# Performance work log

Measured on AMD Instinct MI355X. Metric: run time of the kernel, lower is better.

Reference implementation:

```python
import jax, jax.numpy as jnp
import numpy as np

N_TOKEN = 267735
CUTOFFS = [20000, 40000, 200000, N_TOKEN]  # includes final n_token
D_EMBED = 1024
D_PROJ = 1024
DIV_VAL = 4
N = 1024  # number of tokens


def setup_inputs() -> dict:
    key = jax.random.key(0)
    ks = jax.random.split(key, 20)
    inp = {}
    inp['hidden'] = jax.random.normal(ks[0], (N, D_PROJ), dtype=jnp.float32)
    inp['target'] = jax.random.randint(ks[1], (N,), 0, N_TOKEN, dtype=jnp.int64)
    cutoff_ends = [0] + CUTOFFS
    # per-cluster params: weight [vocab_i, d_emb_i], bias [vocab_i], proj [d_proj, d_emb_i]
    for i in range(4):
        l, r = cutoff_ends[i], cutoff_ends[i + 1]
        d_i = D_EMBED // (DIV_VAL ** i)
        s = 1.0 / np.sqrt(d_i)
        inp[f'W{i}'] = jax.random.uniform(ks[2 + 3 * i], (r - l, d_i), minval=-s, maxval=s, dtype=jnp.float32)
        inp[f'b{i}'] = jnp.zeros((r - l,), dtype=jnp.float32)
        inp[f'proj{i}'] = jax.random.uniform(ks[3 + 3 * i], (D_PROJ, d_i), minval=-s, maxval=s, dtype=jnp.float32)
    inp['cluster_W'] = jax.random.normal(ks[15], (3, D_EMBED), dtype=jnp.float32) * 0.02
    inp['cluster_b'] = jnp.zeros((3,), dtype=jnp.float32)
    return inp


def _adaptive_nll(hidden, target, W0, b0, proj0, W1, b1, proj1, W2, b2, proj2, W3, b3, proj3, cluster_W, cluster_b):
    cutoff_ends = [0] + CUTOFFS
    # head: shortlist vocab + 3 cluster logits
    head_w = jnp.concatenate([W0, cluster_W], axis=0)          # [20003, d_embed]
    head_b = jnp.concatenate([b0, cluster_b], axis=0)          # [20003]
    head_logit = (hidden @ proj0) @ head_w.T + head_b          # [N, 20003]
    head_lp = jax.nn.log_softmax(head_logit, axis=1)
    # shortlist cluster (i == 0)
    t0 = jnp.clip(target, 0, cutoff_ends[1] - 1)
    lp0 = jnp.take_along_axis(head_lp, t0[:, None], axis=1)[:, 0]
    m0 = target < cutoff_ends[1]
    nll = jnp.where(m0, -lp0, 0.0)
    # tail clusters; faithful to original: head column is head_lp[:, -i]
    tails = [(W1, b1, proj1), (W2, b2, proj2), (W3, b3, proj3)]
    for i, (W_i, b_i, proj_i) in enumerate(tails, start=1):
        l, r = cutoff_ends[i], cutoff_ends[i + 1]
        tail_logit = (hidden @ proj_i) @ W_i.T + b_i           # [N, r-l]
        tail_lp = jax.nn.log_softmax(tail_logit, axis=1)
        ti = jnp.clip(target - l, 0, r - l - 1)
        lp_tail = jnp.take_along_axis(tail_lp, ti[:, None], axis=1)[:, 0]
        lp_i = head_lp[:, -i] + lp_tail
        m_i = (target >= l) & (target < r)
        nll = nll + jnp.where(m_i, -lp_i, 0.0)
    return nll.mean()  # reduction='mean'


def reference(hidden, target, W0, b0, proj0, W1, b1, proj1, W2, b2, proj2, W3, b3, proj3, cluster_W, cluster_b):
    return _adaptive_nll(hidden, target, W0, b0, proj0, W1, b1, proj1, W2, b2, proj2, W3, b3, proj3, cluster_W, cluster_b)
```

## Files before the change

### kernel.cpp

```cpp
#include <hip/hip_runtime.h>
#include <stdint.h>


typedef __attribute__((ext_vector_type(8))) short short8;
typedef __attribute__((ext_vector_type(4))) float f32x4;

__device__ __forceinline__ float bf2f(unsigned short u) {
    union { unsigned int i; float f; } v; v.i = ((unsigned int)u) << 16; return v.f;
}
__device__ __forceinline__ unsigned short f2bf(float f) {
    union { float f; unsigned int i; } v; v.f = f;
    unsigned int u = v.i;
    return (unsigned short)((u + 0x7fffu + ((u >> 16) & 1u)) >> 16);
}
__device__ __forceinline__ float wave_sum(float v) {
    v += __shfl_xor(v, 1, 64);  v += __shfl_xor(v, 2, 64);
    v += __shfl_xor(v, 4, 64);  v += __shfl_xor(v, 8, 64);
    v += __shfl_xor(v, 16, 64); v += __shfl_xor(v, 32, 64);
    return v;
}
__device__ __forceinline__ short8 pack8(float4 a, float4 b) {
    union { int4 i; short8 s; } r;
    r.i.x = __builtin_amdgcn_perm(__float_as_uint(a.y), __float_as_uint(a.x), 0x07060302u);
    r.i.y = __builtin_amdgcn_perm(__float_as_uint(a.w), __float_as_uint(a.z), 0x07060302u);
    r.i.z = __builtin_amdgcn_perm(__float_as_uint(b.y), __float_as_uint(b.x), 0x07060302u);
    r.i.w = __builtin_amdgcn_perm(__float_as_uint(b.w), __float_as_uint(b.z), 0x07060302u);
    return r.s;
}

__device__ __forceinline__ void dev_transpose(int bx, int by,
                                              const float* __restrict__ src,
                                              unsigned short* __restrict__ dst,
                                              int K, int N) {
    __shared__ unsigned short tile[32][33];
    int k0 = by * 32, n0 = bx * 32;
    int tx = threadIdx.x & 31, ty = threadIdx.x >> 5;
#pragma unroll
    for (int j = 0; j < 4; ++j) {
        int k = k0 + ty + j * 8, n = n0 + tx;
        float v = (n < N) ? src[(size_t)k * N + n] : 0.f;
        tile[ty + j * 8][tx] = f2bf(v);
    }
    __syncthreads();
#pragma unroll
    for (int j = 0; j < 4; ++j) {
        int n = n0 + ty + j * 8, k = k0 + tx;
        if (n < N) dst[(size_t)n * K + k] = tile[tx][ty + j * 8];
    }
}

__device__ __forceinline__ void dev_biasfill(int bid, const float* __restrict__ b,
                                             float* __restrict__ bp, int vocab, int padded) {
    int i = bid * 256 + threadIdx.x;
    if (i < padded) bp[i] = (i < vocab) ? b[i] : -1e30f;
}

__global__ __launch_bounds__(256)
void k_pre(const float* __restrict__ hidden, unsigned short* __restrict__ hid_bf,
           const float* __restrict__ proj0, unsigned short* __restrict__ pT0,
           const float* __restrict__ proj1, unsigned short* __restrict__ pT1,
           const float* __restrict__ proj2, unsigned short* __restrict__ pT2,
           const float* __restrict__ proj3, unsigned short* __restrict__ pT3,
           const float* __restrict__ b0, float* __restrict__ b0p,
           const float* __restrict__ b1, float* __restrict__ b1p,
           const float* __restrict__ b2, float* __restrict__ b2p,
           const float* __restrict__ b3, float* __restrict__ b3p) {
    int bid = blockIdx.x, tid = threadIdx.x;
    if (bid < 1024) {
        int i = bid * 256 + tid;
        float4 v = ((const float4*)hidden)[i];
        ushort4 o;
        o.x = f2bf(v.x); o.y = f2bf(v.y); o.z = f2bf(v.z); o.w = f2bf(v.w);
        ((ushort4*)hid_bf)[i] = o;
    }
    else if (bid < 2048) { int i = bid - 1024; dev_transpose(i & 31, i >> 5, proj0, pT0, 1024, 1024); }
    else if (bid < 2304) { int i = bid - 2048; dev_transpose(i & 7,  i >> 3, proj1, pT1, 1024, 256); }
    else if (bid < 2368) { int i = bid - 2304; dev_transpose(i & 1,  i >> 1, proj2, pT2, 1024, 64); }
    else if (bid < 2400) { int i = bid - 2368; dev_transpose(0,      i,      proj3, pT3, 1024, 16); }
    else if (bid < 2479) dev_biasfill(bid - 2400, b0, b0p, 20000, 20096);
    else if (bid < 2558) dev_biasfill(bid - 2479, b1, b1p, 20000, 20096);
    else if (bid < 3188) dev_biasfill(bid - 2558, b2, b2p, 160000, 161280);
    else                 dev_biasfill(bid - 3188, b3, b3p, 67735, 69632);
}

template <int NK32, int KD>
__device__ __forceinline__ void dev_convw(int bid, const float* __restrict__ W,
                                          unsigned short* __restrict__ Wf,
                                          int vocab, int upad) {
    int u = bid * 4 + (threadIdx.x >> 6);
    if (u >= upad) return;
    int lane = threadIdx.x & 63, q = lane >> 4, ln = lane & 15;
    int row = u * 16 + ln;
    bool rv = row < vocab;
    const float* src = W + (size_t)row * KD;
#pragma unroll
    for (int ks = 0; ks < NK32; ++ks) {
        int k0 = ks * 32 + q * 8;
        float4 a = {0.f, 0.f, 0.f, 0.f}, b = {0.f, 0.f, 0.f, 0.f};
        if (rv && k0 < KD) {
            a = *(const float4*)(src + k0);
            b = *(const float4*)(src + k0 + 4);
        }
        *(short8*)(Wf + ((size_t)u * NK32 + ks) * 512 + lane * 8) = pack8(a, b);
    }
}

#define BM 128
#define BN 128
#define BK 64
#define LDT 72
template <int NK32O>
__device__ __forceinline__ void dev_gemm(unsigned short* __restrict__ ls,
                                         int bx, int by,
                                         const unsigned short* __restrict__ A, int lda,
                                         const unsigned short* __restrict__ B, int ldb,
                                         unsigned short* __restrict__ Cf,
                                         int N, int K) {
    unsigned short* lsA = ls;
    unsigned short* lsB = ls + BM * LDT;
    int tid = threadIdx.x;
    int mBase = bx * BM, nBase = by * BN;
    int wid = tid >> 6, lane = tid & 63;
    int wr = wid >> 1, wc = wid & 1;
    int q = lane >> 4, ln = lane & 15;
    f32x4 acc[4][4] = {};

    for (int k0 = 0; k0 < K; k0 += BK) {
        __syncthreads();
        int ch = tid & 7;
#pragma unroll
        for (int p = 0; p < 4; ++p) {
            int r = p * 32 + (tid >> 3);
            *(uint4*)(&lsA[r * LDT + ch * 8]) =
                *(const uint4*)(A + (size_t)(mBase + r) * lda + k0 + ch * 8);
        }
#pragma unroll
        for (int p = 0; p < 4; ++p) {
            int r = p * 32 + (tid >> 3);
            uint4 v = {0u, 0u, 0u, 0u};
            if (nBase + r < N)
                v = *(const uint4*)(B + (size_t)(nBase + r) * ldb + k0 + ch * 8);
            *(uint4*)(&lsB[r * LDT + ch * 8]) = v;
        }
        __syncthreads();
#pragma unroll
        for (int ks = 0; ks < 2; ++ks) {
            short8 af[4], bfr[4];
#pragma unroll
            for (int mi = 0; mi < 4; ++mi)
                af[mi] = *(const short8*)(&lsA[(wr * 64 + mi * 16 + ln) * LDT + ks * 32 + q * 8]);
#pragma unroll
            for (int ni = 0; ni < 4; ++ni)
                bfr[ni] = *(const short8*)(&lsB[(wc * 64 + ni * 16 + ln) * LDT + ks * 32 + q * 8]);
#pragma unroll
            for (int mi = 0; mi < 4; ++mi)
#pragma unroll
                for (int ni = 0; ni < 4; ++ni)
                    acc[mi][ni] = __builtin_amdgcn_mfma_f32_16x16x32_bf16(
                        af[mi], bfr[ni], acc[mi][ni], 0, 0, 0);
        }
    }
#pragma unroll
    for (int ni = 0; ni < 4; ++ni) {
        int col = nBase + wc * 64 + ni * 16 + ln;
        if (col < N) {
            int k32 = col >> 5, qc = (col >> 3) & 3, j = col & 7;
#pragma unroll
            for (int mi = 0; mi < 4; ++mi) {
                int m16 = (mBase >> 4) + wr * 4 + mi;
                size_t base = ((size_t)m16 * NK32O + k32) * 512 + (size_t)qc * 128 + j;
#pragma unroll
                for (int r = 0; r < 4; ++r) {
                    int mrem = q * 4 + r;
                    Cf[base + mrem * 8] = f2bf(acc[mi][ni][r]);
                }
            }
        }
    }
}

__global__ __launch_bounds__(256)
void k_mid(const unsigned short* __restrict__ hid_bf,
           const unsigned short* __restrict__ pT0, const unsigned short* __restrict__ pT1,
           const unsigned short* __restrict__ pT2, const unsigned short* __restrict__ pT3,
           unsigned short* __restrict__ h0f, unsigned short* __restrict__ h1f,
           unsigned short* __restrict__ h2f, unsigned short* __restrict__ h3f,
           const float* __restrict__ W0, unsigned short* __restrict__ W0f,
           const float* __restrict__ W1, unsigned short* __restrict__ W1f,
           const float* __restrict__ W2, unsigned short* __restrict__ W2f,
           const float* __restrict__ W3, unsigned short* __restrict__ W3f) {
    __shared__ unsigned short ls[(BM + BN) * LDT];
    int bid = blockIdx.x;
    if (bid < 64)        dev_gemm<32>(ls, bid & 7, bid >> 3, hid_bf, 1024, pT0, 1024, h0f, 1024, 1024);
    else if (bid < 80)   { int i = bid - 64; dev_gemm<8>(ls, i & 7, i >> 3, hid_bf, 1024, pT1, 1024, h1f, 256, 1024); }
    else if (bid < 88)   dev_gemm<2>(ls, bid - 80, 0, hid_bf, 1024, pT2, 1024, h2f, 64, 1024);
    else if (bid < 96)   dev_gemm<1>(ls, bid - 88, 0, hid_bf, 1024, pT3, 1024, h3f, 16, 1024);
    else if (bid < 410)  dev_convw<32, 1024>(bid - 96,   W0, W0f, 20000, 1256);
    else if (bid < 724)  dev_convw<8,  256> (bid - 410,  W1, W1f, 20000, 1256);
    else if (bid < 3244) dev_convw<2,  64>  (bid - 724,  W2, W2f, 160000, 10080);
    else                 dev_convw<1,  16>  (bid - 3244, W3, W3f, 67735, 4352);
}

template <int NK32>
__device__ __forceinline__ void dev_stream(int f,
                const unsigned short* __restrict__ Af,
                const unsigned short* __restrict__ Wf,
                const float* __restrict__ biasp,
                float* __restrict__ rowsum) {
    int u = f & 63;
    int xb = u >> 3;
    int yb = ((f >> 6) << 3) + (u & 7);
    if (yb >= 157) return;

    int tid = threadIdx.x, wid = tid >> 6, lane = tid & 63;
    int wr = wid >> 1, wc = wid & 1;
    int q = lane >> 4, ln = lane & 15;
    int mb = xb * 128 + wr * 64;
    int nb = yb * 128 + wc * 64;

    const unsigned short* Ab = Af + (size_t)(mb >> 4) * NK32 * 512 + lane * 8;
    const unsigned short* Wp[4];
#pragma unroll
    for (int ni = 0; ni < 4; ++ni)
        Wp[ni] = Wf + (size_t)((nb >> 4) + ni) * NK32 * 512 + lane * 8;

    f32x4 acc[4][4] = {};
    short8 a0[4], a1[4], w0[4], w1[4];
    auto LA = [&](short8* d, int kk) {
#pragma unroll
        for (int mi = 0; mi < 4; ++mi)
            d[mi] = *(const short8*)(Ab + ((size_t)mi * NK32 + kk) * 512);
    };
    auto LW = [&](short8* d, int kk) {
#pragma unroll
        for (int ni = 0; ni < 4; ++ni)
            d[ni] = *(const short8*)(Wp[ni] + (size_t)kk * 512);
    };
    auto FM = [&](short8* a, short8* w) {
#pragma unroll
        for (int mi = 0; mi < 4; ++mi)
#pragma unroll
            for (int ni = 0; ni < 4; ++ni)
                acc[mi][ni] = __builtin_amdgcn_mfma_f32_16x16x32_bf16(
                    a[mi], w[ni], acc[mi][ni], 0, 0, 0);
    };

    LA(a0, 0); LW(w0, 0);
#pragma unroll
    for (int ks = 0; ks < NK32; ks += 2) {
        LA(a1, ks + 1); LW(w1, ks + 1);
        FM(a0, w0);
        if (ks + 2 < NK32) { LA(a0, ks + 2); LW(w0, ks + 2); }
        FM(a1, w1);
    }

    float s[4][4];
#pragma unroll
    for (int mi = 0; mi < 4; ++mi)
#pragma unroll
        for (int r = 0; r < 4; ++r) s[mi][r] = 0.f;
#pragma unroll
    for (int ni = 0; ni < 4; ++ni) {
        float b = biasp[nb + ni * 16 + ln];
#pragma unroll
        for (int mi = 0; mi < 4; ++mi)
#pragma unroll
            for (int r = 0; r < 4; ++r)
                s[mi][r] += __expf(acc[mi][ni][r] + b);
    }
#pragma unroll
    for (int mi = 0; mi < 4; ++mi)
#pragma unroll
        for (int r = 0; r < 4; ++r) {
            float v = s[mi][r];
            v += __shfl_xor(v, 1, 64);
            v += __shfl_xor(v, 2, 64);
            v += __shfl_xor(v, 4, 64);
            v += __shfl_xor(v, 8, 64);
            s[mi][r] = v;
        }
    int sl = yb & 31;
    if (ln == 0) {
#pragma unroll
        for (int mi = 0; mi < 4; ++mi)
#pragma unroll
            for (int r = 0; r < 4; ++r)
                atomicAdd(&rowsum[sl * 1024 + mb + mi * 16 + q * 4 + r], s[mi][r]);
    }
}

template <int NK32>
__device__ __forceinline__ void dev_tail(int bx, int by,
                const unsigned short* __restrict__ Af,
                const unsigned short* __restrict__ Wf,
                const float* __restrict__ biasp,
                float* __restrict__ rowsum, int ngroups) {
    int tid = threadIdx.x;
    int wid = tid >> 6, lane = tid & 63;
    int q = lane >> 4, ln = lane & 15;
    int m16b = by * 16 + wid * 4;
    int u0 = bx * ngroups;

    short8 af[4][NK32];
#pragma unroll
    for (int mi = 0; mi < 4; ++mi)
#pragma unroll
        for (int ks = 0; ks < NK32; ++ks)
            af[mi][ks] = *(const short8*)(Af + ((size_t)(m16b + mi) * NK32 + ks) * 512 + lane * 8);

    float rs[4][4];
#pragma unroll
    for (int mi = 0; mi < 4; ++mi)
#pragma unroll
        for (int r = 0; r < 4; ++r) rs[mi][r] = 0.f;

    const unsigned short* Wb = Wf + (size_t)lane * 8;
    auto LWG = [&](short8* d, int u) {
#pragma unroll
        for (int ks = 0; ks < NK32; ++ks)
            d[ks] = *(const short8*)(Wb + ((size_t)u * NK32 + ks) * 512);
    };
    auto CG = [&](short8* w, int u) {
        f32x4 acc[4] = {};
#pragma unroll
        for (int ks = 0; ks < NK32; ++ks)
#pragma unroll
            for (int mi = 0; mi < 4; ++mi)
                acc[mi] = __builtin_amdgcn_mfma_f32_16x16x32_bf16(
                    af[mi][ks], w[ks], acc[mi], 0, 0, 0);
        float b = biasp[u * 16 + ln];
#pragma unroll
        for (int mi = 0; mi < 4; ++mi)
#pragma unroll
            for (int r = 0; r < 4; ++r)
                rs[mi][r] += __expf(acc[mi][r] + b);
    };

    short8 w0[NK32], w1[NK32];
    LWG(w0, u0);
    int g = 0;
    for (; g + 1 < ngroups; g += 2) {
        LWG(w1, u0 + g + 1);
        CG(w0, u0 + g);
        LWG(w0, u0 + g + 2);
        CG(w1, u0 + g + 1);
    }
    if (g < ngroups) CG(w0, u0 + g);

    int sl = bx & 31;
#pragma unroll
    for (int mi = 0; mi < 4; ++mi)
#pragma unroll
        for (int r = 0; r < 4; ++r) {
            float v = rs[mi][r];
            v += __shfl_xor(v, 1, 64);
            v += __shfl_xor(v, 2, 64);
            v += __shfl_xor(v, 4, 64);
            v += __shfl_xor(v, 8, 64);
            if (ln == 0)
                atomicAdd(&rowsum[sl * 1024 + (m16b + mi) * 16 + q * 4 + r], v);
        }
}

__device__ __forceinline__ float frag_dot(const unsigned short* __restrict__ hf,
                                          int NK32, int KdReal, int n,
                                          const float* __restrict__ wrow, int lane) {
    float s = 0.f;
    for (int c = lane; c * 8 < KdReal; c += 64) {
        int k32 = c >> 2, qq = c & 3;
        const unsigned short* p = hf + ((size_t)(n >> 4) * NK32 + k32) * 512 + (qq * 16 + (n & 15)) * 8;
#pragma unroll
        for (int j = 0; j < 8; ++j)
            s += bf2f(p[j]) * wrow[c * 8 + j];
    }
    return wave_sum(s);
}

__device__ __forceinline__ void dev_gather(int bid,
                         const unsigned short* __restrict__ h0f,
                         const unsigned short* __restrict__ h1f,
                         const unsigned short* __restrict__ h2f,
                         const unsigned short* __restrict__ h3f,
                         const float* __restrict__ W0, const float* __restrict__ b0,
                         const float* __restrict__ W1, const float* __restrict__ b1,
                         const float* __restrict__ W2, const float* __restrict__ b2,
                         const float* __restrict__ W3, const float* __restrict__ b3,
                         const float* __restrict__ cW, const float* __restrict__ cb,
                         const int* __restrict__ target,
                         float* __restrict__ rowsum0,
                         float* __restrict__ gat_head,
                         float* __restrict__ gat_tail) {
    int gw = bid * 4 + (threadIdx.x >> 6);
    int lane = threadIdx.x & 63;
    if (gw >= 1024) return;
    int n = gw;
    int t = target[n];

    float cl[3];
#pragma unroll
    for (int j = 0; j < 3; ++j)
        cl[j] = frag_dot(h0f, 32, 1024, n, cW + j * 1024, lane) + cb[j];
    if (lane == 0)
        atomicAdd(&rowsum0[n], __expf(cl[0]) + __expf(cl[1]) + __expf(cl[2]));

    float gh, gt = 0.f;
    if (t < 20000) {
        gh = frag_dot(h0f, 32, 1024, n, W0 + (size_t)t * 1024, lane) + b0[t];
    } else {
        int c, l, Kd, NK32;
        const unsigned short* h; const float* W; const float* b;
        if (t < 40000)       { c = 1; l = 20000;  Kd = 256; NK32 = 8; h = h1f; W = W1; b = b1; }
        else if (t < 200000) { c = 2; l = 40000;  Kd = 64;  NK32 = 2; h = h2f; W = W2; b = b2; }
        else                 { c = 3; l = 200000; Kd = 16;  NK32 = 1; h = h3f; W = W3; b = b3; }
        gh = cl[3 - c];
        gt = frag_dot(h, NK32, Kd, n, W + (size_t)(t - l) * Kd, lane) + b[t - l];
    }
    if (lane == 0) { gat_head[n] = gh; gat_tail[n] = gt; }
}

__global__ __launch_bounds__(256, 2)
void k_logit_all(const unsigned short* __restrict__ h0f, const unsigned short* __restrict__ h1f,
                 const unsigned short* __restrict__ h2f, const unsigned short* __restrict__ h3f,
                 const unsigned short* __restrict__ W0f, const unsigned short* __restrict__ W1f,
                 const unsigned short* __restrict__ W2f, const unsigned short* __restrict__ W3f,
                 const float* __restrict__ b0p, const float* __restrict__ b1p,
                 const float* __restrict__ b2p, const float* __restrict__ b3p,
                 const float* __restrict__ W0, const float* __restrict__ b0,
                 const float* __restrict__ W1, const float* __restrict__ b1,
                 const float* __restrict__ W2, const float* __restrict__ b2,
                 const float* __restrict__ W3, const float* __restrict__ b3,
                 const float* __restrict__ cW, const float* __restrict__ cb,
                 const int* __restrict__ target,
                 float* __restrict__ rowsum,
                 float* __restrict__ gat_head, float* __restrict__ gat_tail) {
    int bid = blockIdx.x;
    if (bid < 1280) {
        dev_stream<32>(bid, h0f, W0f, b0p, rowsum);
    } else if (bid < 2560) {
        dev_stream<8>(bid - 1280, h1f, W1f, b1p, rowsum + 32768);
    } else if (bid < 3200) {
        int i = bid - 2560;
        dev_tail<2>(i % 160, i / 160, h2f, W2f, b2p, rowsum + 65536, 63);
    } else if (bid < 3712) {
        int i = bid - 3200;
        dev_tail<1>(i & 127, i >> 7, h3f, W3f, b3p, rowsum + 98304, 34);
    } else {
        dev_gather(bid - 3712, h0f, h1f, h2f, h3f, W0, b0, W1, b1, W2, b2, W3, b3,
                   cW, cb, target, rowsum, gat_head, gat_tail);
    }
}

__global__ void k_finalize(const float* __restrict__ rs,
                           const float* __restrict__ gat_head,
                           const float* __restrict__ gat_tail,
                           const int* __restrict__ target,
                           float* __restrict__ out) {
    __shared__ float red[16];
    int n = threadIdx.x;
    int t = target[n];
    float r0 = 0.f;
#pragma unroll
    for (int s = 0; s < 32; ++s) r0 += rs[s * 1024 + n];
    float nll = __logf(r0) - gat_head[n];
    int c = (t < 20000) ? 0 : (t < 40000) ? 1 : (t < 200000) ? 2 : 3;
    if (c > 0) {
        float rc = 0.f;
#pragma unroll
        for (int s = 0; s < 32; ++s) rc += rs[c * 32768 + s * 1024 + n];
        nll += __logf(rc) - gat_tail[n];
    }
    float sm = wave_sum(nll);
    int wid = n >> 6, lane = n & 63;
    if (lane == 0) red[wid] = sm;
    __syncthreads();
    if (n == 0) {
        float tot = 0.f;
#pragma unroll
        for (int i = 0; i < 16; ++i) tot += red[i];
        out[0] = tot / 1024.0f;
    }
}

extern "C" void kernel_launch(void* const* d_in, const int* in_sizes, int n_in,
                              void* d_out, int out_size, void* d_ws, size_t ws_size,
                              hipStream_t stream) {
    const float* hidden = (const float*)d_in[0];
    const int*   target = (const int*)d_in[1];
    const float* W0 = (const float*)d_in[2];
    const float* b0 = (const float*)d_in[3];
    const float* proj0 = (const float*)d_in[4];
    const float* W1 = (const float*)d_in[5];
    const float* b1 = (const float*)d_in[6];
    const float* proj1 = (const float*)d_in[7];
    const float* W2 = (const float*)d_in[8];
    const float* b2 = (const float*)d_in[9];
    const float* proj2 = (const float*)d_in[10];
    const float* W3 = (const float*)d_in[11];
    const float* b3 = (const float*)d_in[12];
    const float* proj3 = (const float*)d_in[13];
    const float* cW = (const float*)d_in[14];
    const float* cb = (const float*)d_in[15];

    char* ws = (char*)d_ws;
    unsigned short* hid_bf = (unsigned short*)(ws + 0x000000);
    unsigned short* pT0 = (unsigned short*)(ws + 0x200000);
    unsigned short* pT1 = (unsigned short*)(ws + 0x400000);
    unsigned short* pT2 = (unsigned short*)(ws + 0x480000);
    unsigned short* pT3 = (unsigned short*)(ws + 0x4A0000);
    unsigned short* h0f = (unsigned short*)(ws + 0x4A8000);
    unsigned short* h1f = (unsigned short*)(ws + 0x6A8000);
    unsigned short* h2f = (unsigned short*)(ws + 0x728000);
    unsigned short* h3f = (unsigned short*)(ws + 0x748000);
    float* rowsum   = (float*)(ws + 0x758000);
    float* gat_head = (float*)(ws + 0x7D8000);
    float* gat_tail = (float*)(ws + 0x7D9000);
    unsigned short* W0f = (unsigned short*)(ws + 0x00800000);
    unsigned short* W1f = (unsigned short*)(ws + 0x02F40000);
    unsigned short* W2f = (unsigned short*)(ws + 0x03910000);
    unsigned short* W3f = (unsigned short*)(ws + 0x04CC0000);
    float* b0p = (float*)(ws + 0x05100000);
    float* b1p = (float*)(ws + 0x05114000);
    float* b2p = (float*)(ws + 0x05128000);
    float* b3p = (float*)(ws + 0x051C8000);

    hipMemsetAsync(ws + 0x748000, 0, 0x92000, stream);

    k_pre<<<3460, 256, 0, stream>>>(hidden, hid_bf,
                                    proj0, pT0, proj1, pT1, proj2, pT2, proj3, pT3,
                                    b0, b0p, b1, b1p, b2, b2p, b3, b3p);

    k_mid<<<4332, 256, 0, stream>>>(hid_bf, pT0, pT1, pT2, pT3, h0f, h1f, h2f, h3f,
                                    W0, W0f, W1, W1f, W2, W2f, W3, W3f);

    k_logit_all<<<3968, 256, 0, stream>>>(h0f, h1f, h2f, h3f, W0f, W1f, W2f, W3f,
                                          b0p, b1p, b2p, b3p,
                                          W0, b0, W1, b1, W2, b2, W3, b3,
                                          cW, cb, target, rowsum, gat_head, gat_tail);

    k_finalize<<<1, 1024, 0, stream>>>(rowsum, gat_head, gat_tail, target, (float*)d_out);
}
```

Measured before the change: 395.4 us.

## Fuse fp32-to-bf16 weight conversion into logit GEMM loads

```diff
diff --git a/kernel.cpp b/kernel.cpp
--- a/kernel.cpp
+++ b/kernel.cpp
@@ -81,28 +81,6 @@
     else if (bid < 2558) dev_biasfill(bid - 2479, b1, b1p, 20000, 20096);
     else if (bid < 3188) dev_biasfill(bid - 2558, b2, b2p, 160000, 161280);
     else                 dev_biasfill(bid - 3188, b3, b3p, 67735, 69632);
-}
-
-template <int NK32, int KD>
-__device__ __forceinline__ void dev_convw(int bid, const float* __restrict__ W,
-                                          unsigned short* __restrict__ Wf,
-                                          int vocab, int upad) {
-    int u = bid * 4 + (threadIdx.x >> 6);
-    if (u >= upad) return;
-    int lane = threadIdx.x & 63, q = lane >> 4, ln = lane & 15;
-    int row = u * 16 + ln;
-    bool rv = row < vocab;
-    const float* src = W + (size_t)row * KD;
-#pragma unroll
-    for (int ks = 0; ks < NK32; ++ks) {
-        int k0 = ks * 32 + q * 8;
-        float4 a = {0.f, 0.f, 0.f, 0.f}, b = {0.f, 0.f, 0.f, 0.f};
-        if (rv && k0 < KD) {
-            a = *(const float4*)(src + k0);
-            b = *(const float4*)(src + k0 + 4);
-        }
-        *(short8*)(Wf + ((size_t)u * NK32 + ks) * 512 + lane * 8) = pack8(a, b);
-    }
 }
 
 #define BM 128
@@ -180,33 +158,25 @@
 }
 
 __global__ __launch_bounds__(256)
-void k_mid(const unsigned short* __restrict__ hid_bf,
-           const unsigned short* __restrict__ pT0, const unsigned short* __restrict__ pT1,
-           const unsigned short* __restrict__ pT2, const unsigned short* __restrict__ pT3,
-           unsigned short* __restrict__ h0f, unsigned short* __restrict__ h1f,
-           unsigned short* __restrict__ h2f, unsigned short* __restrict__ h3f,
-           const float* __restrict__ W0, unsigned short* __restrict__ W0f,
-           const float* __restrict__ W1, unsigned short* __restrict__ W1f,
-           const float* __restrict__ W2, unsigned short* __restrict__ W2f,
-           const float* __restrict__ W3, unsigned short* __restrict__ W3f) {
+void k_gemm_all(const unsigned short* __restrict__ hid_bf,
+                const unsigned short* __restrict__ pT0, const unsigned short* __restrict__ pT1,
+                const unsigned short* __restrict__ pT2, const unsigned short* __restrict__ pT3,
+                unsigned short* __restrict__ h0f, unsigned short* __restrict__ h1f,
+                unsigned short* __restrict__ h2f, unsigned short* __restrict__ h3f) {
     __shared__ unsigned short ls[(BM + BN) * LDT];
     int bid = blockIdx.x;
-    if (bid < 64)        dev_gemm<32>(ls, bid & 7, bid >> 3, hid_bf, 1024, pT0, 1024, h0f, 1024, 1024);
-    else if (bid < 80)   { int i = bid - 64; dev_gemm<8>(ls, i & 7, i >> 3, hid_bf, 1024, pT1, 1024, h1f, 256, 1024); }
-    else if (bid < 88)   dev_gemm<2>(ls, bid - 80, 0, hid_bf, 1024, pT2, 1024, h2f, 64, 1024);
-    else if (bid < 96)   dev_gemm<1>(ls, bid - 88, 0, hid_bf, 1024, pT3, 1024, h3f, 16, 1024);
-    else if (bid < 410)  dev_convw<32, 1024>(bid - 96,   W0, W0f, 20000, 1256);
-    else if (bid < 724)  dev_convw<8,  256> (bid - 410,  W1, W1f, 20000, 1256);
-    else if (bid < 3244) dev_convw<2,  64>  (bid - 724,  W2, W2f, 160000, 10080);
-    else                 dev_convw<1,  16>  (bid - 3244, W3, W3f, 67735, 4352);
-}
-
-template <int NK32>
+    if (bid < 64)      dev_gemm<32>(ls, bid & 7, bid >> 3, hid_bf, 1024, pT0, 1024, h0f, 1024, 1024);
+    else if (bid < 80) { int i = bid - 64; dev_gemm<8>(ls, i & 7, i >> 3, hid_bf, 1024, pT1, 1024, h1f, 256, 1024); }
+    else if (bid < 88) dev_gemm<2>(ls, bid - 80, 0, hid_bf, 1024, pT2, 1024, h2f, 64, 1024);
+    else               dev_gemm<1>(ls, bid - 88, 0, hid_bf, 1024, pT3, 1024, h3f, 16, 1024);
+}
+
+template <int NK32, int KD>
 __device__ __forceinline__ void dev_stream(int f,
                 const unsigned short* __restrict__ Af,
-                const unsigned short* __restrict__ Wf,
+                const float* __restrict__ W,
                 const float* __restrict__ biasp,
-                float* __restrict__ rowsum) {
+                float* __restrict__ rowsum, int vocabm1) {
     int u = f & 63;
     int xb = u >> 3;
     int yb = ((f >> 6) << 3) + (u & 7);
@@ -219,22 +189,31 @@
     int nb = yb * 128 + wc * 64;
 
     const unsigned short* Ab = Af + (size_t)(mb >> 4) * NK32 * 512 + lane * 8;
-    const unsigned short* Wp[4];
-#pragma unroll
-    for (int ni = 0; ni < 4; ++ni)
-        Wp[ni] = Wf + (size_t)((nb >> 4) + ni) * NK32 * 512 + lane * 8;
+    const float* Wp[4];
+#pragma unroll
+    for (int ni = 0; ni < 4; ++ni) {
+        int rw = min(nb + ni * 16 + ln, vocabm1);
+        Wp[ni] = W + (size_t)rw * KD + q * 8;
+    }
 
     f32x4 acc[4][4] = {};
     short8 a0[4], a1[4], w0[4], w1[4];
+    float4 fa[4], fb[4];
     auto LA = [&](short8* d, int kk) {
 #pragma unroll
         for (int mi = 0; mi < 4; ++mi)
             d[mi] = *(const short8*)(Ab + ((size_t)mi * NK32 + kk) * 512);
     };
-    auto LW = [&](short8* d, int kk) {
-#pragma unroll
-        for (int ni = 0; ni < 4; ++ni)
-            d[ni] = *(const short8*)(Wp[ni] + (size_t)kk * 512);
+    auto LWF = [&](int kk) {
+#pragma unroll
+        for (int ni = 0; ni < 4; ++ni) {
+            fa[ni] = *(const float4*)(Wp[ni] + kk * 32);
+            fb[ni] = *(const float4*)(Wp[ni] + kk * 32 + 4);
+        }
+    };
+    auto PK = [&](short8* d) {
+#pragma unroll
+        for (int ni = 0; ni < 4; ++ni) d[ni] = pack8(fa[ni], fb[ni]);
     };
     auto FM = [&](short8* a, short8* w) {
 #pragma unroll
@@ -245,13 +224,15 @@
                     a[mi], w[ni], acc[mi][ni], 0, 0, 0);
     };
 
-    LA(a0, 0); LW(w0, 0);
+    LA(a0, 0); LWF(0); PK(w0);
 #pragma unroll
     for (int ks = 0; ks < NK32; ks += 2) {
-        LA(a1, ks + 1); LW(w1, ks + 1);
+        LA(a1, ks + 1); LWF(ks + 1);
         FM(a0, w0);
-        if (ks + 2 < NK32) { LA(a0, ks + 2); LW(w0, ks + 2); }
+        PK(w1);
+        if (ks + 2 < NK32) { LA(a0, ks + 2); LWF(ks + 2); }
         FM(a1, w1);
+        if (ks + 2 < NK32) PK(w0);
     }
 
     float s[4][4];
@@ -289,12 +270,12 @@
     }
 }
 
-template <int NK32>
+template <int NK32, int KDR>
 __device__ __forceinline__ void dev_tail(int bx, int by,
                 const unsigned short* __restrict__ Af,
-                const unsigned short* __restrict__ Wf,
+                const float* __restrict__ W,
                 const float* __restrict__ biasp,
-                float* __restrict__ rowsum, int ngroups) {
+                float* __restrict__ rowsum, int ngroups, int vocabm1) {
     int tid = threadIdx.x;
     int wid = tid >> 6, lane = tid & 63;
     int q = lane >> 4, ln = lane & 15;
@@ -314,11 +295,20 @@
 #pragma unroll
         for (int r = 0; r < 4; ++r) rs[mi][r] = 0.f;
 
-    const unsigned short* Wb = Wf + (size_t)lane * 8;
-    auto LWG = [&](short8* d, int u) {
-#pragma unroll
-        for (int ks = 0; ks < NK32; ++ks)
-            d[ks] = *(const short8*)(Wb + ((size_t)u * NK32 + ks) * 512);
+    float4 fa[NK32], fb[NK32];
+    auto LWF = [&](int u) {
+        int rw = min(u * 16 + ln, vocabm1);
+        const float* p = W + (size_t)rw * KDR + q * 8;
+        if constexpr (KDR == 16) {
+            if (q < 2) { fa[0] = *(const float4*)p; fb[0] = *(const float4*)(p + 4); }
+            else       { fa[0] = float4{0,0,0,0};   fb[0] = float4{0,0,0,0}; }
+        } else {
+#pragma unroll
+            for (int ks = 0; ks < NK32; ++ks) {
+                fa[ks] = *(const float4*)(p + ks * 32);
+                fb[ks] = *(const float4*)(p + ks * 32 + 4);
+            }
+        }
     };
     auto CG = [&](short8* w, int u) {
         f32x4 acc[4] = {};
@@ -336,16 +326,24 @@
                 rs[mi][r] += __expf(acc[mi][r] + b);
     };
 
-    short8 w0[NK32], w1[NK32];
-    LWG(w0, u0);
+    short8 wA[NK32], wB[NK32];
+    LWF(u0);
+#pragma unroll
+    for (int ks = 0; ks < NK32; ++ks) wA[ks] = pack8(fa[ks], fb[ks]);
     int g = 0;
-    for (; g + 1 < ngroups; g += 2) {
-        LWG(w1, u0 + g + 1);
-        CG(w0, u0 + g);
-        LWG(w0, u0 + g + 2);
-        CG(w1, u0 + g + 1);
-    }
-    if (g < ngroups) CG(w0, u0 + g);
+    for (; g + 2 <= ngroups; g += 2) {
+        LWF(u0 + g + 1);
+        CG(wA, u0 + g);
+#pragma unroll
+        for (int ks = 0; ks < NK32; ++ks) wB[ks] = pack8(fa[ks], fb[ks]);
+        if (g + 2 < ngroups) LWF(u0 + g + 2);
+        CG(wB, u0 + g + 1);
+        if (g + 2 < ngroups) {
+#pragma unroll
+            for (int ks = 0; ks < NK32; ++ks) wA[ks] = pack8(fa[ks], fb[ks]);
+        }
+    }
+    if (g < ngroups) CG(wA, u0 + g);
 
     int sl = bx & 31;
 #pragma unroll
@@ -421,8 +419,6 @@
 __global__ __launch_bounds__(256, 2)
 void k_logit_all(const unsigned short* __restrict__ h0f, const unsigned short* __restrict__ h1f,
                  const unsigned short* __restrict__ h2f, const unsigned short* __restrict__ h3f,
-                 const unsigned short* __restrict__ W0f, const unsigned short* __restrict__ W1f,
-                 const unsigned short* __restrict__ W2f, const unsigned short* __restrict__ W3f,
                  const float* __restrict__ b0p, const float* __restrict__ b1p,
                  const float* __restrict__ b2p, const float* __restrict__ b3p,
                  const float* __restrict__ W0, const float* __restrict__ b0,
@@ -435,15 +431,15 @@
                  float* __restrict__ gat_head, float* __restrict__ gat_tail) {
     int bid = blockIdx.x;
     if (bid < 1280) {
-        dev_stream<32>(bid, h0f, W0f, b0p, rowsum);
+        dev_stream<32, 1024>(bid, h0f, W0, b0p, rowsum, 19999);
     } else if (bid < 2560) {
-        dev_stream<8>(bid - 1280, h1f, W1f, b1p, rowsum + 32768);
+        dev_stream<8, 256>(bid - 1280, h1f, W1, b1p, rowsum + 32768, 19999);
     } else if (bid < 3200) {
         int i = bid - 2560;
-        dev_tail<2>(i % 160, i / 160, h2f, W2f, b2p, rowsum + 65536, 63);
+        dev_tail<2, 64>(i % 160, i / 160, h2f, W2, b2p, rowsum + 65536, 63, 159999);
     } else if (bid < 3712) {
         int i = bid - 3200;
-        dev_tail<1>(i & 127, i >> 7, h3f, W3f, b3p, rowsum + 98304, 34);
+        dev_tail<1, 16>(i & 127, i >> 7, h3f, W3, b3p, rowsum + 98304, 34, 67734);
     } else {
         dev_gather(bid - 3712, h0f, h1f, h2f, h3f, W0, b0, W1, b1, W2, b2, W3, b3,
                    cW, cb, target, rowsum, gat_head, gat_tail);
@@ -514,10 +510,6 @@
     float* rowsum   = (float*)(ws + 0x758000);
     float* gat_head = (float*)(ws + 0x7D8000);
     float* gat_tail = (float*)(ws + 0x7D9000);
-    unsigned short* W0f = (unsigned short*)(ws + 0x00800000);
-    unsigned short* W1f = (unsigned short*)(ws + 0x02F40000);
-    unsigned short* W2f = (unsigned short*)(ws + 0x03910000);
-    unsigned short* W3f = (unsigned short*)(ws + 0x04CC0000);
     float* b0p = (float*)(ws + 0x05100000);
     float* b1p = (float*)(ws + 0x05114000);
     float* b2p = (float*)(ws + 0x05128000);
@@ -529,10 +521,9 @@
                                     proj0, pT0, proj1, pT1, proj2, pT2, proj3, pT3,
                                     b0, b0p, b1, b1p, b2, b2p, b3, b3p);
 
-    k_mid<<<4332, 256, 0, stream>>>(hid_bf, pT0, pT1, pT2, pT3, h0f, h1f, h2f, h3f,
-                                    W0, W0f, W1, W1f, W2, W2f, W3, W3f);
-
-    k_logit_all<<<3968, 256, 0, stream>>>(h0f, h1f, h2f, h3f, W0f, W1f, W2f, W3f,
+    k_gemm_all<<<96, 256, 0, stream>>>(hid_bf, pT0, pT1, pT2, pT3, h0f, h1f, h2f, h3f);
+
+    k_logit_all<<<3968, 256, 0, stream>>>(h0f, h1f, h2f, h3f,
                                           b0p, b1p, b2p, b3p,
                                           W0, b0, W1, b1, W2, b2, W3, b3,
                                           cW, cb, target, rowsum, gat_head, gat_tail);
```

Measured after the change: 614.5 us. 55.4% more time.
